# Kernel optimization log

Hardware: AMD Instinct MI355X
Metric: run time of the kernel (lower is better)

Reference implementation:

```python
import jax, jax.numpy as jnp
import numpy as np

BIG = 1e10


def setup_inputs() -> dict:
    key = jax.random.key(0)
    k1, k2, k3, k4 = jax.random.split(key, 4)
    B, N = 8, 4096
    pred = jax.random.normal(k1, (B, N, 3), dtype=jnp.float32)
    target = jax.random.normal(k2, (B, N, 3), dtype=jnp.float32)
    points = jax.random.normal(k3, (B, N, 3), dtype=jnp.float32)
    mask = jax.random.randint(k4, (B, N), 0, 2, dtype=jnp.int32)
    return {"pred": pred, "target": target, "mask": mask, "points": points}


def reference(pred, target, mask, points):
    # clean / predicted point clouds: points plus residual displacements
    clean = points + target          # [B, N, 3]
    predp = points + pred            # [B, N, 3]
    m = mask.astype(bool)            # [B, N] validity mask (same mask for both sets)

    # (avoids materializing a [B, N, N, 3] difference tensor).
    x2 = jnp.sum(clean * clean, axis=-1)                    # [B, N]
    y2 = jnp.sum(predp * predp, axis=-1)                    # [B, N]
    xy = jnp.einsum('bnd,bmd->bnm', clean, predp)           # [B, N, N]
    d = jnp.maximum(x2[:, :, None] + y2[:, None, :] - 2.0 * xy, 0.0)  # [B, N, N]

    # For each clean point (row), nearest valid pred point: mask invalid columns.
    min_x = jnp.min(jnp.where(m[:, None, :], d, BIG), axis=2)  # [B, N]
    # For each pred point (col), nearest valid clean point: mask invalid rows.
    min_y = jnp.min(jnp.where(m[:, :, None], d, BIG), axis=1)  # [B, N]

    cnt = jnp.sum(m, axis=1).astype(jnp.float32)                # valid points per sample
    cham_x = jnp.sum(jnp.where(m, min_x, 0.0), axis=1) / cnt    # point_reduction='mean'
    cham_y = jnp.sum(jnp.where(m, min_y, 0.0), axis=1) / cnt

    # batch_reduction='sum' across samples, then divide by number of batches
    B = mask.shape[0]
    return jnp.sum(cham_x + cham_y) / B
```

## Files before the change

kernel.cpp:

```cpp
#include <hip/hip_runtime.h>

#define NPTS 4096
#define BATCH 8
#define BIGF 1e10f

typedef __attribute__((ext_vector_type(8))) short short8;
typedef __attribute__((ext_vector_type(4))) float f32x4;
typedef unsigned short us;

__device__ __forceinline__ us trbf(float f) { return (us)(__float_as_uint(f) >> 16); }
__device__ __forceinline__ float bff(us s)  { return __uint_as_float(((unsigned)s) << 16); }
__device__ __forceinline__ void split3(float v, us* h, us* m, us* l) {
    *h = trbf(v); float r1 = v - bff(*h);
    *m = trbf(r1); float r2 = r1 - bff(*m);
    *l = trbf(r2);
}
__device__ __forceinline__ unsigned pk2(us a, us b) { return (unsigned)a | ((unsigned)b << 16); }

__device__ __forceinline__ void apack(float x, float y, float z,
                                      uint4* __restrict__ dst, int r) {
    const us one = 0x3F80;
    us thx,tmx,tlx, thy,tmy,tly, thz,tmz,tlz, x2h,x2m,x2l;
    split3(-2.f*x,&thx,&tmx,&tlx);
    split3(-2.f*y,&thy,&tmy,&tly);
    split3(-2.f*z,&thz,&tmz,&tlz);
    split3(x*x + y*y + z*z,&x2h,&x2m,&x2l);
    us ak[24] = {thx,thy,thz, thx,thy,thz, thx,thy,thz,
                 tmx,tmy,tmz, tmx,tmy,tmz, tlx,tly,tlz,
                 x2h,x2m,x2l, one,one,one};
#pragma unroll
    for (int gg = 0; gg < 3; gg++)
        dst[gg*16+r] = make_uint4(pk2(ak[gg*8+0],ak[gg*8+1]), pk2(ak[gg*8+2],ak[gg*8+3]),
                                  pk2(ak[gg*8+4],ak[gg*8+5]), pk2(ak[gg*8+6],ak[gg*8+7]));
    dst[48+r] = make_uint4(0,0,0,0);
}

__device__ __forceinline__ void bpack(
    const float* __restrict__ points, const float* __restrict__ bres,
    const int* __restrict__ mask, int g, uint4* __restrict__ dst, int r)
{
    float x = points[g*3+0] + bres[g*3+0];
    float y = points[g*3+1] + bres[g*3+1];
    float z = points[g*3+2] + bres[g*3+2];
    float wq = x*x + y*y + z*z + (mask[g] ? 0.f : BIGF);
    const us one = 0x3F80;
    us bhx,bmx,blx, bhy,bmy,bly, bhz,bmz,blz, wh,wm,wl;
    split3(x,&bhx,&bmx,&blx);
    split3(y,&bhy,&bmy,&bly);
    split3(z,&bhz,&bmz,&blz);
    split3(wq,&wh,&wm,&wl);
    us bk[24] = {bhx,bhy,bhz, bmx,bmy,bmz, blx,bly,blz,
                 bhx,bhy,bhz, bmx,bmy,bmz, bhx,bhy,bhz,
                 one,one,one, wh,wm,wl};
#pragma unroll
    for (int gg = 0; gg < 3; gg++)
        dst[gg*16+r] = make_uint4(pk2(bk[gg*8+0],bk[gg*8+1]), pk2(bk[gg*8+2],bk[gg*8+3]),
                                  pk2(bk[gg*8+4],bk[gg*8+5]), pk2(bk[gg*8+6],bk[gg*8+7]));
    dst[48+r] = make_uint4(0,0,0,0);
}

__global__ __launch_bounds__(512, 4) void fused_kernel(
    const float* __restrict__ pred, const float* __restrict__ target,
    const int* __restrict__ mask, const float* __restrict__ points,
    float* __restrict__ out)
{
    __shared__ uint4 Bsh[2][2048];
    __shared__ uint4 Ash[512];
    __shared__ float scnt[8], swave[8];

    int bid = blockIdx.x;
    int strip = bid & 31, b = (bid >> 5) & 7, dir = bid >> 8;
    int t = threadIdx.x, w = t >> 6, lane = t & 63;

    const float* __restrict__ ares = dir ? pred : target;
    const float* __restrict__ bres = dir ? target : pred;

    if (t < 128) {
        int g = b * NPTS + strip * 128 + t;
        float x = points[g*3+0] + ares[g*3+0];
        float y = points[g*3+1] + ares[g*3+1];
        float z = points[g*3+2] + ares[g*3+2];
        apack(x, y, z, Ash + (t >> 4) * 64, t & 15);
    }
    bpack(points, bres, mask, b * NPTS + t, &Bsh[0][(t >> 4) * 64], t & 15);

    int csum = 0;
    const int4* m4 = (const int4*)(mask + b * NPTS);
#pragma unroll
    for (int r = 0; r < 2; r++) { int4 v = m4[r * 512 + t]; csum += v.x + v.y + v.z + v.w; }
#pragma unroll
    for (int s = 32; s; s >>= 1) csum += __shfl_down(csum, s, 64);
    if (lane == 0) scnt[w] = (float)csum;

    f32x4 rm = {3e38f,3e38f,3e38f,3e38f};
    f32x4 zero = {0.f,0.f,0.f,0.f};

    __syncthreads();

    short8 Af = ((const short8*)Ash)[w * 64 + lane];

    for (int c = 0; c < 8; c++) {
        int nb = c & 1;
        if (c < 7)
            bpack(points, bres, mask, b * NPTS + (c + 1) * 512 + t,
                  &Bsh[nb ^ 1][(t >> 4) * 64], t & 15);
        const short8* Bt = (const short8*)&Bsh[nb][0];
#pragma unroll
        for (int p = 0; p < 16; p++) {
            short8 b0 = Bt[(2 * p + 0) * 64 + lane];
            short8 b1 = Bt[(2 * p + 1) * 64 + lane];
            f32x4 d0 = __builtin_amdgcn_mfma_f32_16x16x32_bf16(Af, b0, zero, 0, 0, 0);
            f32x4 d1 = __builtin_amdgcn_mfma_f32_16x16x32_bf16(Af, b1, zero, 0, 0, 0);
#pragma unroll
            for (int j = 0; j < 4; j++)
                rm[j] = fminf(fminf(rm[j], d0[j]), d1[j]);
        }
        __syncthreads();
    }

#pragma unroll
    for (int s = 1; s <= 8; s <<= 1) {
        f32x4 o;
#pragma unroll
        for (int j = 0; j < 4; j++) o[j] = __shfl_xor(rm[j], s, 64);
#pragma unroll
        for (int j = 0; j < 4; j++) rm[j] = fminf(rm[j], o[j]);
    }
    float part = 0.f;
    if ((lane & 15) == 0) {
        int g = lane >> 4;
        int rowbase = b * NPTS + strip * 128 + w * 16 + g * 4;
#pragma unroll
        for (int j = 0; j < 4; j++)
            if (mask[rowbase + j]) part += fmaxf(rm[j], 0.f);
    }
    part += __shfl_xor(part, 16, 64);
    part += __shfl_xor(part, 32, 64);
    if (lane == 0) swave[w] = part;
    __syncthreads();
    if (t == 0) {
        float C = 0.f, S = 0.f;
#pragma unroll
        for (int i = 0; i < 8; i++) { C += scnt[i]; S += swave[i]; }
        atomicAdd(out, S / C * 0.125f);
    }
}

extern "C" void kernel_launch(void* const* d_in, const int* in_sizes, int n_in,
                              void* d_out, int out_size, void* d_ws, size_t ws_size,
                              hipStream_t stream) {
    const float* pred   = (const float*)d_in[0];
    const float* target = (const float*)d_in[1];
    const int*   mask   = (const int*)d_in[2];
    const float* points = (const float*)d_in[3];
    float* out = (float*)d_out;

    hipMemsetAsync(out, 0, sizeof(float), stream);
    fused_kernel<<<512, 512, 0, stream>>>(pred, target, mask, points, out);
}
```

Baseline: 31.80 us.

## Switch to 32x32x16 MFMA with 2-term bf16 split and larger row strips

Replaces the 16x16x32 MFMA distance tiles with 32x32x16 MFMA tiles. Each wave now covers 32 rows, so a block handles 256 query rows and the grid halves to 256 blocks. The three-way bf16 split of coordinates is reduced to a round-to-nearest two-way split, which packs the K dimension into 16 elements and cuts the MFMA work per output element. The aim is less matrix and packing work per distance. The cost is lower precision in the distance expansion, 16 accumulator registers per lane, and fewer blocks to spread across the CUs.

```diff
diff --git a/kernel.cpp b/kernel.cpp
--- a/kernel.cpp
+++ b/kernel.cpp
@@ -5,84 +5,73 @@
 #define BIGF 1e10f
 
 typedef __attribute__((ext_vector_type(8))) short short8;
-typedef __attribute__((ext_vector_type(4))) float f32x4;
+typedef __attribute__((ext_vector_type(16))) float f32x16;
 typedef unsigned short us;
 
-__device__ __forceinline__ us trbf(float f) { return (us)(__float_as_uint(f) >> 16); }
-__device__ __forceinline__ float bff(us s)  { return __uint_as_float(((unsigned)s) << 16); }
-__device__ __forceinline__ void split3(float v, us* h, us* m, us* l) {
-    *h = trbf(v); float r1 = v - bff(*h);
-    *m = trbf(r1); float r2 = r1 - bff(*m);
-    *l = trbf(r2);
+__device__ __forceinline__ us f2bf(float f) {
+    unsigned u = __float_as_uint(f);
+    return (us)((u + 0x7FFFu + ((u >> 16) & 1u)) >> 16);
+}
+__device__ __forceinline__ float bff(us s) { return __uint_as_float(((unsigned)s) << 16); }
+__device__ __forceinline__ void split2(float v, us* h, us* m) {
+    *h = f2bf(v); *m = f2bf(v - bff(*h));
 }
 __device__ __forceinline__ unsigned pk2(us a, us b) { return (unsigned)a | ((unsigned)b << 16); }
 
-__device__ __forceinline__ void apack(float x, float y, float z,
-                                      uint4* __restrict__ dst, int r) {
+__device__ __forceinline__ void apackA(float x, float y, float z,
+                                       uint4* __restrict__ dst, int row) {
     const us one = 0x3F80;
-    us thx,tmx,tlx, thy,tmy,tly, thz,tmz,tlz, x2h,x2m,x2l;
-    split3(-2.f*x,&thx,&tmx,&tlx);
-    split3(-2.f*y,&thy,&tmy,&tly);
-    split3(-2.f*z,&thz,&tmz,&tlz);
-    split3(x*x + y*y + z*z,&x2h,&x2m,&x2l);
-    us ak[24] = {thx,thy,thz, thx,thy,thz, thx,thy,thz,
-                 tmx,tmy,tmz, tmx,tmy,tmz, tlx,tly,tlz,
-                 x2h,x2m,x2l, one,one,one};
-#pragma unroll
-    for (int gg = 0; gg < 3; gg++)
-        dst[gg*16+r] = make_uint4(pk2(ak[gg*8+0],ak[gg*8+1]), pk2(ak[gg*8+2],ak[gg*8+3]),
-                                  pk2(ak[gg*8+4],ak[gg*8+5]), pk2(ak[gg*8+6],ak[gg*8+7]));
-    dst[48+r] = make_uint4(0,0,0,0);
+    us thx,tmx, thy,tmy, thz,tmz, x2h,x2m;
+    split2(-2.f*x, &thx,&tmx);
+    split2(-2.f*y, &thy,&tmy);
+    split2(-2.f*z, &thz,&tmz);
+    split2(x*x + y*y + z*z, &x2h,&x2m);
+    dst[row]      = make_uint4(pk2(thx,thy), pk2(thz,thx), pk2(thy,thz), pk2(tmx,tmy));
+    dst[row + 32] = make_uint4(pk2(tmz,x2h), pk2(x2m,one), pk2(one,0),   pk2(0,0));
 }
 
-__device__ __forceinline__ void bpack(
+__device__ __forceinline__ void bpackB(
     const float* __restrict__ points, const float* __restrict__ bres,
-    const int* __restrict__ mask, int g, uint4* __restrict__ dst, int r)
+    const int* __restrict__ mask, int g, uint4* __restrict__ dst, int col)
 {
     float x = points[g*3+0] + bres[g*3+0];
     float y = points[g*3+1] + bres[g*3+1];
     float z = points[g*3+2] + bres[g*3+2];
     float wq = x*x + y*y + z*z + (mask[g] ? 0.f : BIGF);
     const us one = 0x3F80;
-    us bhx,bmx,blx, bhy,bmy,bly, bhz,bmz,blz, wh,wm,wl;
-    split3(x,&bhx,&bmx,&blx);
-    split3(y,&bhy,&bmy,&bly);
-    split3(z,&bhz,&bmz,&blz);
-    split3(wq,&wh,&wm,&wl);
-    us bk[24] = {bhx,bhy,bhz, bmx,bmy,bmz, blx,bly,blz,
-                 bhx,bhy,bhz, bmx,bmy,bmz, bhx,bhy,bhz,
-                 one,one,one, wh,wm,wl};
-#pragma unroll
-    for (int gg = 0; gg < 3; gg++)
-        dst[gg*16+r] = make_uint4(pk2(bk[gg*8+0],bk[gg*8+1]), pk2(bk[gg*8+2],bk[gg*8+3]),
-                                  pk2(bk[gg*8+4],bk[gg*8+5]), pk2(bk[gg*8+6],bk[gg*8+7]));
-    dst[48+r] = make_uint4(0,0,0,0);
+    us bhx,bmx, bhy,bmy, bhz,bmz, wh,wm;
+    split2(x, &bhx,&bmx);
+    split2(y, &bhy,&bmy);
+    split2(z, &bhz,&bmz);
+    split2(wq, &wh,&wm);
+    dst[col]      = make_uint4(pk2(bhx,bhy), pk2(bhz,bmx), pk2(bmy,bmz), pk2(bhx,bhy));
+    dst[col + 32] = make_uint4(pk2(bhz,one), pk2(one,wh),  pk2(wm,0),    pk2(0,0));
 }
 
-__global__ __launch_bounds__(512, 4) void fused_kernel(
+__global__ __launch_bounds__(512, 2) void fused_kernel(
     const float* __restrict__ pred, const float* __restrict__ target,
     const int* __restrict__ mask, const float* __restrict__ points,
     float* __restrict__ out)
 {
-    __shared__ uint4 Bsh[2][2048];
-    __shared__ uint4 Ash[512];
+    __shared__ uint4 Bsh[2][16][64];
+    __shared__ uint4 Ash[8][64];
     __shared__ float scnt[8], swave[8];
 
     int bid = blockIdx.x;
-    int strip = bid & 31, b = (bid >> 5) & 7, dir = bid >> 8;
+    int strip = bid & 15, b = (bid >> 4) & 7, dir = bid >> 7;
     int t = threadIdx.x, w = t >> 6, lane = t & 63;
 
     const float* __restrict__ ares = dir ? pred : target;
     const float* __restrict__ bres = dir ? target : pred;
 
-    if (t < 128) {
-        int g = b * NPTS + strip * 128 + t;
+    if (t < 256) {
+        int g = b * NPTS + strip * 256 + t;
         float x = points[g*3+0] + ares[g*3+0];
         float y = points[g*3+1] + ares[g*3+1];
         float z = points[g*3+2] + ares[g*3+2];
-        apack(x, y, z, Ash + (t >> 4) * 64, t & 15);
+        apackA(x, y, z, &Ash[t >> 5][0], t & 31);
     }
-    bpack(points, bres, mask, b * NPTS + t, &Bsh[0][(t >> 4) * 64], t & 15);
+    bpackB(points, bres, mask, b * NPTS + t, &Bsh[0][t >> 5][0], t & 31);
 
     int csum = 0;
     const int4* m4 = (const int4*)(mask + b * NPTS);
@@ -92,8 +81,10 @@
     for (int s = 32; s; s >>= 1) csum += __shfl_down(csum, s, 64);
     if (lane == 0) scnt[w] = (float)csum;
 
-    f32x4 rm = {3e38f,3e38f,3e38f,3e38f};
-    f32x4 zero = {0.f,0.f,0.f,0.f};
+    float rm[16];
+#pragma unroll
+    for (int r = 0; r < 16; r++) rm[r] = 3e38f;
+    f32x16 zero = {0.f,0.f,0.f,0.f,0.f,0.f,0.f,0.f,0.f,0.f,0.f,0.f,0.f,0.f,0.f,0.f};
 
     __syncthreads();
 
@@ -102,39 +93,38 @@
     for (int c = 0; c < 8; c++) {
         int nb = c & 1;
         if (c < 7)
-            bpack(points, bres, mask, b * NPTS + (c + 1) * 512 + t,
-                  &Bsh[nb ^ 1][(t >> 4) * 64], t & 15);
-        const short8* Bt = (const short8*)&Bsh[nb][0];
+            bpackB(points, bres, mask, b * NPTS + (c + 1) * 512 + t,
+                   &Bsh[nb ^ 1][t >> 5][0], t & 31);
+        const short8* Bt = (const short8*)&Bsh[nb][0][0];
 #pragma unroll
-        for (int p = 0; p < 16; p++) {
-            short8 b0 = Bt[(2 * p + 0) * 64 + lane];
-            short8 b1 = Bt[(2 * p + 1) * 64 + lane];
-            f32x4 d0 = __builtin_amdgcn_mfma_f32_16x16x32_bf16(Af, b0, zero, 0, 0, 0);
-            f32x4 d1 = __builtin_amdgcn_mfma_f32_16x16x32_bf16(Af, b1, zero, 0, 0, 0);
+        for (int p = 0; p < 16; p += 2) {
+            short8 b0 = Bt[(p + 0) * 64 + lane];
+            short8 b1 = Bt[(p + 1) * 64 + lane];
+            f32x16 d0 = __builtin_amdgcn_mfma_f32_32x32x16_bf16(Af, b0, zero, 0, 0, 0);
+            f32x16 d1 = __builtin_amdgcn_mfma_f32_32x32x16_bf16(Af, b1, zero, 0, 0, 0);
 #pragma unroll
-            for (int j = 0; j < 4; j++)
-                rm[j] = fminf(fminf(rm[j], d0[j]), d1[j]);
+            for (int r = 0; r < 16; r++)
+                rm[r] = fminf(fminf(rm[r], d0[r]), d1[r]);
         }
         __syncthreads();
     }
 
 #pragma unroll
-    for (int s = 1; s <= 8; s <<= 1) {
-        f32x4 o;
+    for (int r = 0; r < 16; r++) {
 #pragma unroll
-        for (int j = 0; j < 4; j++) o[j] = __shfl_xor(rm[j], s, 64);
-#pragma unroll
-        for (int j = 0; j < 4; j++) rm[j] = fminf(rm[j], o[j]);
+        for (int s = 1; s <= 16; s <<= 1)
+            rm[r] = fminf(rm[r], __shfl_xor(rm[r], s, 64));
     }
     float part = 0.f;
-    if ((lane & 15) == 0) {
-        int g = lane >> 4;
-        int rowbase = b * NPTS + strip * 128 + w * 16 + g * 4;
+    if ((lane & 31) == 0) {
+        int h = lane >> 5;
+        int rowbase = b * NPTS + strip * 256 + w * 32 + 4 * h;
 #pragma unroll
-        for (int j = 0; j < 4; j++)
-            if (mask[rowbase + j]) part += fmaxf(rm[j], 0.f);
+        for (int r = 0; r < 16; r++) {
+            int row = rowbase + (r & 3) + 8 * (r >> 2);
+            if (mask[row]) part += fmaxf(rm[r], 0.f);
+        }
     }
-    part += __shfl_xor(part, 16, 64);
     part += __shfl_xor(part, 32, 64);
     if (lane == 0) swave[w] = part;
     __syncthreads();
@@ -156,5 +146,5 @@
     float* out = (float*)d_out;
 
     hipMemsetAsync(out, 0, sizeof(float), stream);
-    fused_kernel<<<512, 512, 0, stream>>>(pred, target, mask, points, out);
+    fused_kernel<<<256, 512, 0, stream>>>(pred, target, mask, points, out);
 }
```

Result: faster. 26.35 us, median of 2 (-17.1%).
